# Performance work log

Hardware: AMD Instinct MI355X
Metric: run time of the kernel (lower is better)

## Reference

```python
import jax, jax.numpy as jnp
import numpy as np

BOUNDS = 1.6
N_PTS = 1_000_000
FEAT = 32
RES = 512


def _sample_plane(plane, coords):
    """Bilinear grid_sample, align_corners=True, border padding.
    plane: [C, H, W]; coords: [N, 2] with (x, y) in [-1, 1] (x -> W, y -> H).
    Returns [N, C].
    """
    C, H, W = plane.shape
    x = jnp.clip((coords[:, 0] + 1.0) * 0.5 * (W - 1), 0.0, W - 1)
    y = jnp.clip((coords[:, 1] + 1.0) * 0.5 * (H - 1), 0.0, H - 1)
    x0 = jnp.floor(x)
    y0 = jnp.floor(y)
    wx = x - x0
    wy = y - y0
    x0i = x0.astype(jnp.int32)
    y0i = y0.astype(jnp.int32)
    x1i = jnp.minimum(x0i + 1, W - 1)
    y1i = jnp.minimum(y0i + 1, H - 1)
    # gathers -> [C, N]
    v00 = plane[:, y0i, x0i]
    v01 = plane[:, y0i, x1i]
    v10 = plane[:, y1i, x0i]
    v11 = plane[:, y1i, x1i]
    out = (v00 * ((1 - wx) * (1 - wy)) + v01 * (wx * (1 - wy))
           + v10 * ((1 - wx) * wy) + v11 * (wx * wy))
    return out.T  # [N, C]


def setup_inputs() -> dict:
    key = jax.random.key(0)
    k1, k2, k3 = jax.random.split(key, 3)
    pts = jax.random.normal(k1, (N_PTS, 3), dtype=jnp.float32)
    time = jax.random.uniform(k2, (N_PTS, 1), dtype=jnp.float32)
    planes = jax.random.normal(k3, (6, FEAT, RES, RES), dtype=jnp.float32) * 0.1
    return {"pts": pts, "time": time, "planes": planes, "scales": 1}


def reference(pts, time, planes, scales):
    # normalize_aabb: aabb = [[b,b,b],[-b,-b,-b]] -> map to [-1, 1]
    aabb_max = jnp.float32(BOUNDS)
    aabb_min = jnp.float32(-BOUNDS)
    pts_n = (pts - aabb_min) / (aabb_max - aabb_min) * 2.0 - 1.0
    pts_n = pts_n.reshape(-1, pts_n.shape[-1])
    t = time * 2.0 - 1.0
    data = jnp.concatenate([pts_n, t], axis=-1)  # [N, 4]
    # plane order 0..5 with the (q,r) / (r,q) index swaps from the source:
    # i=0 (0,1) space | i=1 (0,2) space | i=2 (3,0) spacetime
    # i=3 (1,2) space | i=4 (3,1) spacetime | i=5 (3,2) spacetime
    idx = jnp.array([[0, 1], [0, 2], [3, 0], [1, 2], [3, 1], [3, 2]])
    coords = data[:, idx]                 # [N, 6, 2]
    coords = jnp.transpose(coords, (1, 0, 2))  # [6, N, 2]
    feats = jax.vmap(_sample_plane)(planes, coords)  # [6, N, C]
    space = feats[0] * feats[1] * feats[3]
    spacetime = feats[2] * feats[4] * feats[5]
    return space, spacetime
```

## Files before the change

### kernel.cpp

```cpp
#include <hip/hip_runtime.h>
#include <hip/hip_fp16.h>

#define RES 512
#define FEAT 32
#define NPLANES 6
#define XT 128
#define TP (XT + 4)

__global__ __launch_bounds__(256) void transpose_fp16_kernel(
    const float* __restrict__ in, __half* __restrict__ out)
{
    __shared__ float tile[FEAT][TP];
    const int b  = blockIdx.x;
    const int xt = b & 3;
    const int y  = (b >> 2) & (RES - 1);
    const int p  = b >> 11;
    const int xbase = xt << 7;

    const size_t pb = (size_t)p * ((size_t)FEAT * RES * RES) + (size_t)y * RES + xbase;
    #pragma unroll
    for (int j = 0; j < 4; ++j) {
        const int f  = threadIdx.x + j * 256;
        const int c  = f >> 5;
        const int x4 = (f & 31) << 2;
        const float4 v = *(const float4*)(in + pb + (size_t)c * (RES * RES) + x4);
        *(float4*)&tile[c][x4] = v;
    }
    __syncthreads();

    const int m  = threadIdx.x >> 1;
    const int c0 = (threadIdx.x & 1) << 4;
    union { __half h[16]; float4 f4[2]; } u;
    #pragma unroll
    for (int j = 0; j < 16; ++j)
        u.h[j] = __float2half_rn(tile[c0 + j][m]);

    const size_t ob = (((size_t)p * RES + y) * RES + xbase) * FEAT
                    + (size_t)threadIdx.x * 16;
    *(float4*)(out + ob)     = u.f4[0];
    *(float4*)(out + ob + 8) = u.f4[1];
}

__device__ __forceinline__ void unpack8(const float4 r, float* o)
{
    const __half2* h = (const __half2*)&r;
    float2 p;
    p = __half22float2(h[0]); o[0] = p.x; o[1] = p.y;
    p = __half22float2(h[1]); o[2] = p.x; o[3] = p.y;
    p = __half22float2(h[2]); o[4] = p.x; o[5] = p.y;
    p = __half22float2(h[3]); o[6] = p.x; o[7] = p.y;
}

template <int XIq, int YIq, int Q>
__device__ __forceinline__ void sample_plane(
    const float* d, const __half* __restrict__ planes, int sub, float* f)
{
    const float u = d[XIq];
    const float v = d[YIq];
    float fx = fminf(fmaxf((u + 1.0f) * 0.5f * 511.0f, 0.0f), 511.0f);
    float fy = fminf(fmaxf((v + 1.0f) * 0.5f * 511.0f, 0.0f), 511.0f);
    const float x0f = floorf(fx), y0f = floorf(fy);
    const float wx = fx - x0f,   wy = fy - y0f;
    const int x0 = (int)x0f, y0 = (int)y0f;
    const int x1 = min(x0 + 1, RES - 1), y1 = min(y0 + 1, RES - 1);
    const float w00 = (1.0f - wx) * (1.0f - wy);
    const float w01 = wx * (1.0f - wy);
    const float w10 = (1.0f - wx) * wy;
    const float w11 = wx * wy;

    const __half* P = planes + ((size_t)Q << 23) + (sub << 3);
    const int r0 = y0 << 9, r1 = y1 << 9;
    const float4 a00 = *(const float4*)(P + ((size_t)(r0 + x0) << 5));
    const float4 a01 = *(const float4*)(P + ((size_t)(r0 + x1) << 5));
    const float4 a10 = *(const float4*)(P + ((size_t)(r1 + x0) << 5));
    const float4 a11 = *(const float4*)(P + ((size_t)(r1 + x1) << 5));

    float v00[8], v01[8], v10[8], v11[8];
    unpack8(a00, v00); unpack8(a01, v01); unpack8(a10, v10); unpack8(a11, v11);
    #pragma unroll
    for (int i = 0; i < 8; ++i)
        f[i] = v00[i] * w00 + v01[i] * w01 + v10[i] * w10 + v11[i] * w11;
}

__global__ __launch_bounds__(256) void sample_fp16_kernel(
    const float* __restrict__ pts, const float* __restrict__ tm,
    const __half* __restrict__ planes, float* __restrict__ out, int npts)
{
    const int t  = blockIdx.x * 256 + threadIdx.x;
    const int pt = t >> 2;
    const int sub = t & 3;
    if (pt >= npts) return;

    float d[4];
    d[0] = (pts[(size_t)pt * 3 + 0] + 1.6f) / 3.2f * 2.0f - 1.0f;
    d[1] = (pts[(size_t)pt * 3 + 1] + 1.6f) / 3.2f * 2.0f - 1.0f;
    d[2] = (pts[(size_t)pt * 3 + 2] + 1.6f) / 3.2f * 2.0f - 1.0f;
    d[3] = tm[pt] * 2.0f - 1.0f;

    float f[8], sp[8], st[8];

    sample_plane<0, 1, 0>(d, planes, sub, sp);
    sample_plane<0, 2, 1>(d, planes, sub, f);
    #pragma unroll
    for (int i = 0; i < 8; ++i) sp[i] *= f[i];
    sample_plane<1, 2, 3>(d, planes, sub, f);
    #pragma unroll
    for (int i = 0; i < 8; ++i) sp[i] *= f[i];
    {
        float4* o = (float4*)(out + (size_t)pt * FEAT + (sub << 3));
        o[0] = *(float4*)&sp[0];
        o[1] = *(float4*)&sp[4];
    }

    sample_plane<3, 0, 2>(d, planes, sub, st);
    sample_plane<3, 1, 4>(d, planes, sub, f);
    #pragma unroll
    for (int i = 0; i < 8; ++i) st[i] *= f[i];
    sample_plane<3, 2, 5>(d, planes, sub, f);
    #pragma unroll
    for (int i = 0; i < 8; ++i) st[i] *= f[i];
    {
        float4* o = (float4*)(out + (size_t)npts * FEAT + (size_t)pt * FEAT + (sub << 3));
        o[0] = *(float4*)&st[0];
        o[1] = *(float4*)&st[4];
    }
}

__global__ __launch_bounds__(256) void sample_fallback_kernel(
    const float* __restrict__ pts, const float* __restrict__ tm,
    const float* __restrict__ planes, float* __restrict__ out, int npts)
{
    const int t  = blockIdx.x * 256 + threadIdx.x;
    const int pt = t >> 5;
    const int c  = t & 31;
    if (pt >= npts) return;

    float d[4];
    d[0] = (pts[(size_t)pt * 3 + 0] + 1.6f) / 3.2f * 2.0f - 1.0f;
    d[1] = (pts[(size_t)pt * 3 + 1] + 1.6f) / 3.2f * 2.0f - 1.0f;
    d[2] = (pts[(size_t)pt * 3 + 2] + 1.6f) / 3.2f * 2.0f - 1.0f;
    d[3] = tm[pt] * 2.0f - 1.0f;

    const int xi[NPLANES] = {0, 0, 3, 1, 3, 3};
    const int yi[NPLANES] = {1, 2, 0, 2, 1, 2};
    float f[NPLANES];
    #pragma unroll
    for (int q = 0; q < NPLANES; ++q) {
        const float u = d[xi[q]], v = d[yi[q]];
        float fx = fminf(fmaxf((u + 1.0f) * 0.5f * 511.0f, 0.0f), 511.0f);
        float fy = fminf(fmaxf((v + 1.0f) * 0.5f * 511.0f, 0.0f), 511.0f);
        const float x0f = floorf(fx), y0f = floorf(fy);
        const float wx = fx - x0f, wy = fy - y0f;
        const int x0 = (int)x0f, y0 = (int)y0f;
        const int x1 = min(x0 + 1, RES - 1), y1 = min(y0 + 1, RES - 1);
        const float* P = planes + ((size_t)(q * FEAT + c) << 18);
        const int r0 = y0 << 9, r1 = y1 << 9;
        f[q] = P[r0 + x0] * ((1.0f - wx) * (1.0f - wy)) + P[r0 + x1] * (wx * (1.0f - wy)) +
               P[r1 + x0] * ((1.0f - wx) * wy)          + P[r1 + x1] * (wx * wy);
    }
    out[(size_t)pt * FEAT + c] = f[0] * f[1] * f[3];
    out[(size_t)npts * FEAT + (size_t)pt * FEAT + c] = f[2] * f[4] * f[5];
}

extern "C" void kernel_launch(void* const* d_in, const int* in_sizes, int n_in,
                              void* d_out, int out_size, void* d_ws, size_t ws_size,
                              hipStream_t stream) {
    const float* pts    = (const float*)d_in[0];
    const float* tm     = (const float*)d_in[1];
    const float* planes = (const float*)d_in[2];
    float* out = (float*)d_out;
    const int npts = in_sizes[0] / 3;

    const size_t need = (size_t)NPLANES * FEAT * RES * RES * sizeof(__half);
    if (ws_size >= need) {
        __half* T = (__half*)d_ws;
        transpose_fp16_kernel<<<NPLANES * RES * 4, 256, 0, stream>>>(planes, T);
        const int blocks = (npts * 4 + 255) / 256;
        sample_fp16_kernel<<<blocks, 256, 0, stream>>>(pts, tm, T, out, npts);
    } else {
        const int blocks = (npts * 32 + 255) / 256;
        sample_fallback_kernel<<<blocks, 256, 0, stream>>>(pts, tm, planes, out, npts);
    }
}
```

Before: 711.5 us.

## Batch all 24 plane gathers before interpolation and widen fp16 transpose tiles

The sampling kernel now computes all six planes' offsets and weights up front and issues all 24 vectorized gathers before doing any interpolation. This exposes more memory-level parallelism instead of serializing load-then-compute per plane. The transpose kernel now handles a full row per block, converts to fp16 before writing to shared memory, and uses nontemporal loads for the fp32 source. The cost is much higher register pressure in the sampler (24 float4 values live at once), which may reduce occupancy.

Result: faster. 688.4 us (-3.2%).

```diff
diff --git a/kernel.cpp b/kernel.cpp
--- a/kernel.cpp
+++ b/kernel.cpp
@@ -4,41 +4,49 @@
 #define RES 512
 #define FEAT 32
 #define NPLANES 6
-#define XT 128
-#define TP (XT + 4)
+#define TPH (RES + 8)
+
+typedef float f4 __attribute__((ext_vector_type(4)));
 
 __global__ __launch_bounds__(256) void transpose_fp16_kernel(
     const float* __restrict__ in, __half* __restrict__ out)
 {
-    __shared__ float tile[FEAT][TP];
-    const int b  = blockIdx.x;
-    const int xt = b & 3;
-    const int y  = (b >> 2) & (RES - 1);
-    const int p  = b >> 11;
-    const int xbase = xt << 7;
+    __shared__ __half tile[FEAT][TPH];
+    const int b = blockIdx.x;
+    const int y = b & (RES - 1);
+    const int p = b >> 9;
 
-    const size_t pb = (size_t)p * ((size_t)FEAT * RES * RES) + (size_t)y * RES + xbase;
+    const size_t pb = (size_t)p * ((size_t)FEAT * RES * RES) + (size_t)y * RES;
     #pragma unroll
-    for (int j = 0; j < 4; ++j) {
+    for (int j = 0; j < 16; ++j) {
         const int f  = threadIdx.x + j * 256;
-        const int c  = f >> 5;
-        const int x4 = (f & 31) << 2;
-        const float4 v = *(const float4*)(in + pb + (size_t)c * (RES * RES) + x4);
-        *(float4*)&tile[c][x4] = v;
+        const int c  = f >> 7;
+        const int x4 = (f & 127) << 2;
+        const f4 v = __builtin_nontemporal_load(
+            (const f4*)(in + pb + (size_t)c * (RES * RES) + x4));
+        union { __half h[4]; float2 f2; } u;
+        u.h[0] = __float2half_rn(v[0]);
+        u.h[1] = __float2half_rn(v[1]);
+        u.h[2] = __float2half_rn(v[2]);
+        u.h[3] = __float2half_rn(v[3]);
+        *(float2*)&tile[c][x4] = u.f2;
     }
     __syncthreads();
 
-    const int m  = threadIdx.x >> 1;
+    const int xl = threadIdx.x >> 1;
     const int c0 = (threadIdx.x & 1) << 4;
-    union { __half h[16]; float4 f4[2]; } u;
+    const size_t ob0 = ((size_t)(p * RES + y) * RES) * FEAT + c0;
     #pragma unroll
-    for (int j = 0; j < 16; ++j)
-        u.h[j] = __float2half_rn(tile[c0 + j][m]);
-
-    const size_t ob = (((size_t)p * RES + y) * RES + xbase) * FEAT
-                    + (size_t)threadIdx.x * 16;
-    *(float4*)(out + ob)     = u.f4[0];
-    *(float4*)(out + ob + 8) = u.f4[1];
+    for (int it = 0; it < 4; ++it) {
+        const int x = xl + (it << 7);
+        union { __half h[16]; float4 q[2]; } u;
+        #pragma unroll
+        for (int j = 0; j < 16; ++j)
+            u.h[j] = tile[c0 + j][x];
+        __half* o = out + ob0 + (size_t)x * FEAT;
+        *(float4*)o       = u.q[0];
+        *(float4*)(o + 8) = u.q[1];
+    }
 }
 
 __device__ __forceinline__ void unpack8(const float4 r, float* o)
@@ -49,37 +57,6 @@
     p = __half22float2(h[1]); o[2] = p.x; o[3] = p.y;
     p = __half22float2(h[2]); o[4] = p.x; o[5] = p.y;
     p = __half22float2(h[3]); o[6] = p.x; o[7] = p.y;
-}
-
-template <int XIq, int YIq, int Q>
-__device__ __forceinline__ void sample_plane(
-    const float* d, const __half* __restrict__ planes, int sub, float* f)
-{
-    const float u = d[XIq];
-    const float v = d[YIq];
-    float fx = fminf(fmaxf((u + 1.0f) * 0.5f * 511.0f, 0.0f), 511.0f);
-    float fy = fminf(fmaxf((v + 1.0f) * 0.5f * 511.0f, 0.0f), 511.0f);
-    const float x0f = floorf(fx), y0f = floorf(fy);
-    const float wx = fx - x0f,   wy = fy - y0f;
-    const int x0 = (int)x0f, y0 = (int)y0f;
-    const int x1 = min(x0 + 1, RES - 1), y1 = min(y0 + 1, RES - 1);
-    const float w00 = (1.0f - wx) * (1.0f - wy);
-    const float w01 = wx * (1.0f - wy);
-    const float w10 = (1.0f - wx) * wy;
-    const float w11 = wx * wy;
-
-    const __half* P = planes + ((size_t)Q << 23) + (sub << 3);
-    const int r0 = y0 << 9, r1 = y1 << 9;
-    const float4 a00 = *(const float4*)(P + ((size_t)(r0 + x0) << 5));
-    const float4 a01 = *(const float4*)(P + ((size_t)(r0 + x1) << 5));
-    const float4 a10 = *(const float4*)(P + ((size_t)(r1 + x0) << 5));
-    const float4 a11 = *(const float4*)(P + ((size_t)(r1 + x1) << 5));
-
-    float v00[8], v01[8], v10[8], v11[8];
-    unpack8(a00, v00); unpack8(a01, v01); unpack8(a10, v10); unpack8(a11, v11);
-    #pragma unroll
-    for (int i = 0; i < 8; ++i)
-        f[i] = v00[i] * w00 + v01[i] * w01 + v10[i] * w10 + v11[i] * w11;
 }
 
 __global__ __launch_bounds__(256) void sample_fp16_kernel(
@@ -97,32 +74,66 @@
     d[2] = (pts[(size_t)pt * 3 + 2] + 1.6f) / 3.2f * 2.0f - 1.0f;
     d[3] = tm[pt] * 2.0f - 1.0f;
 
-    float f[8], sp[8], st[8];
+    const int xi[NPLANES] = {0, 0, 3, 1, 3, 3};
+    const int yi[NPLANES] = {1, 2, 0, 2, 1, 2};
 
-    sample_plane<0, 1, 0>(d, planes, sub, sp);
-    sample_plane<0, 2, 1>(d, planes, sub, f);
+    int   off[NPLANES][4];
+    float w[NPLANES][4];
     #pragma unroll
-    for (int i = 0; i < 8; ++i) sp[i] *= f[i];
-    sample_plane<1, 2, 3>(d, planes, sub, f);
+    for (int q = 0; q < NPLANES; ++q) {
+        const float u = d[xi[q]];
+        const float v = d[yi[q]];
+        float fx = fminf(fmaxf((u + 1.0f) * 0.5f * 511.0f, 0.0f), 511.0f);
+        float fy = fminf(fmaxf((v + 1.0f) * 0.5f * 511.0f, 0.0f), 511.0f);
+        const float x0f = floorf(fx), y0f = floorf(fy);
+        const float wx = fx - x0f,   wy = fy - y0f;
+        const int x0 = (int)x0f, y0 = (int)y0f;
+        const int x1 = min(x0 + 1, RES - 1), y1 = min(y0 + 1, RES - 1);
+        const int r0 = y0 << 9, r1 = y1 << 9;
+        off[q][0] = (r0 + x0) << 5;
+        off[q][1] = (r0 + x1) << 5;
+        off[q][2] = (r1 + x0) << 5;
+        off[q][3] = (r1 + x1) << 5;
+        w[q][0] = (1.0f - wx) * (1.0f - wy);
+        w[q][1] = wx * (1.0f - wy);
+        w[q][2] = (1.0f - wx) * wy;
+        w[q][3] = wx * wy;
+    }
+
+    float4 a[NPLANES][4];
     #pragma unroll
-    for (int i = 0; i < 8; ++i) sp[i] *= f[i];
+    for (int q = 0; q < NPLANES; ++q) {
+        const __half* P = planes + ((size_t)q << 23) + (sub << 3);
+        #pragma unroll
+        for (int k = 0; k < 4; ++k)
+            a[q][k] = *(const float4*)(P + off[q][k]);
+    }
+
+    float fq[NPLANES][8];
+    #pragma unroll
+    for (int q = 0; q < NPLANES; ++q) {
+        float v00[8], v01[8], v10[8], v11[8];
+        unpack8(a[q][0], v00); unpack8(a[q][1], v01);
+        unpack8(a[q][2], v10); unpack8(a[q][3], v11);
+        #pragma unroll
+        for (int i = 0; i < 8; ++i)
+            fq[q][i] = v00[i] * w[q][0] + v01[i] * w[q][1]
+                     + v10[i] * w[q][2] + v11[i] * w[q][3];
+    }
+
     {
+        float sp[8], st[8];
+        #pragma unroll
+        for (int i = 0; i < 8; ++i) {
+            sp[i] = fq[0][i] * fq[1][i] * fq[3][i];
+            st[i] = fq[2][i] * fq[4][i] * fq[5][i];
+        }
         float4* o = (float4*)(out + (size_t)pt * FEAT + (sub << 3));
         o[0] = *(float4*)&sp[0];
         o[1] = *(float4*)&sp[4];
-    }
-
-    sample_plane<3, 0, 2>(d, planes, sub, st);
-    sample_plane<3, 1, 4>(d, planes, sub, f);
-    #pragma unroll
-    for (int i = 0; i < 8; ++i) st[i] *= f[i];
-    sample_plane<3, 2, 5>(d, planes, sub, f);
-    #pragma unroll
-    for (int i = 0; i < 8; ++i) st[i] *= f[i];
-    {
-        float4* o = (float4*)(out + (size_t)npts * FEAT + (size_t)pt * FEAT + (sub << 3));
-        o[0] = *(float4*)&st[0];
-        o[1] = *(float4*)&st[4];
+        float4* o2 = (float4*)(out + (size_t)npts * FEAT + (size_t)pt * FEAT + (sub << 3));
+        o2[0] = *(float4*)&st[0];
+        o2[1] = *(float4*)&st[4];
     }
 }
 
@@ -174,7 +185,7 @@
     const size_t need = (size_t)NPLANES * FEAT * RES * RES * sizeof(__half);
     if (ws_size >= need) {
         __half* T = (__half*)d_ws;
-        transpose_fp16_kernel<<<NPLANES * RES * 4, 256, 0, stream>>>(planes, T);
+        transpose_fp16_kernel<<<NPLANES * RES, 256, 0, stream>>>(planes, T);
         const int blocks = (npts * 4 + 255) / 256;
         sample_fp16_kernel<<<blocks, 256, 0, stream>>>(pts, tm, T, out, npts);
     } else {
```
